# Kernel tuning notes

Hardware: AMD Instinct MI355X
Metric: run time of the kernel (lower is better)

Reference implementation:

```python
import jax, jax.numpy as jnp
import numpy as np

B, T, H, NH, L, V, FF = 2, 1024, 1024, 16, 6, 8192, 4096
D = H // NH
EPS = 1e-5


def _ln(x, g, b):
    mu = jnp.mean(x, axis=-1, keepdims=True)
    var = jnp.mean(jnp.square(x - mu), axis=-1, keepdims=True)
    return (x - mu) * jax.lax.rsqrt(var + EPS) * g + b


def setup_inputs() -> dict:
    key = jax.random.key(0)
    ks = jax.random.split(key, 12)
    s = 1.0 / np.sqrt(H)
    return {
        "x": jax.random.randint(ks[0], (B, T), 0, V),
        "tok_emb": jax.random.normal(ks[1], (V, H), jnp.float32) * s,
        "pos_emb": jax.random.normal(ks[2], (1, T, H), jnp.float32) * s,
        "Wq": jax.random.normal(ks[3], (L, H, H), jnp.float32) * s,
        "bq": jnp.zeros((L, H), jnp.float32),
        "Wk": jax.random.normal(ks[4], (L, H, H), jnp.float32) * s,
        "bk": jnp.zeros((L, H), jnp.float32),
        "Wv": jax.random.normal(ks[5], (L, H, H), jnp.float32) * s,
        "bv": jnp.zeros((L, H), jnp.float32),
        "Wo": jax.random.normal(ks[6], (L, H, H), jnp.float32) * s,
        "bo": jnp.zeros((L, H), jnp.float32),
        "W1": jax.random.normal(ks[7], (L, H, FF), jnp.float32) * s,
        "b1": jnp.zeros((L, FF), jnp.float32),
        "W2": jax.random.normal(ks[8], (L, FF, H), jnp.float32) * (1.0 / np.sqrt(FF)),
        "b2": jnp.zeros((L, H), jnp.float32),
        "ln1_g": jnp.ones((L, H), jnp.float32),
        "ln1_b": jnp.zeros((L, H), jnp.float32),
        "ln2_g": jnp.ones((L, H), jnp.float32),
        "ln2_b": jnp.zeros((L, H), jnp.float32),
        "lnf_g": jnp.ones((H,), jnp.float32),
        "lnf_b": jnp.zeros((H,), jnp.float32),
        "headW": jax.random.normal(ks[9], (H, V), jnp.float32) * s,
        "headb": jnp.zeros((V,), jnp.float32),
    }


def _transformer(x, tok_emb, pos_emb, Wq, bq, Wk, bk, Wv, bv, Wo, bo,
                 W1, b1, W2, b2, ln1_g, ln1_b, ln2_g, ln2_b, lnf_g, lnf_b,
                 headW, headb):
    Tcur = x.shape[1]
    h = tok_emb[x] + pos_emb[:, :Tcur, :]            # [B,T,H]
    mask = jnp.tril(jnp.ones((Tcur, Tcur), bool))    # causal [T,T]
    scale = 1.0 / np.sqrt(D)

    def block(h, p):
        (wq, q_b, wk, k_b, wv, v_b, wo, o_b,
         w1, b1_, w2, b2_, g1, be1, g2, be2) = p
        q = (h @ wq + q_b).reshape(B, Tcur, NH, D)
        k = (h @ wk + k_b).reshape(B, Tcur, NH, D)
        v = (h @ wv + v_b).reshape(B, Tcur, NH, D)
        att = jnp.einsum('bqnd,bknd->bnqk', q, k) * scale
        att = jnp.where(mask, att, -jnp.inf)
        w = jax.nn.softmax(att, axis=-1)
        o = jnp.einsum('bnqk,bknd->bqnd', w, v).reshape(B, Tcur, H)
        h = _ln(h + (o @ wo + o_b), g1, be1)          # post-LN after attention
        m = jax.nn.gelu(h @ w1 + b1_, approximate=False) @ w2 + b2_
        h = _ln(h + m, g2, be2)                       # post-LN after MLP
        return h, None

    params = (Wq, bq, Wk, bk, Wv, bv, Wo, bo, W1, b1, W2, b2,
              ln1_g, ln1_b, ln2_g, ln2_b)
    h, _ = jax.lax.scan(block, h, params)
    h = _ln(h, lnf_g, lnf_b)
    return h @ headW + headb                          # [B,T,V]


def reference(x, tok_emb, pos_emb, Wq, bq, Wk, bk, Wv, bv, Wo, bo,
              W1, b1, W2, b2, ln1_g, ln1_b, ln2_g, ln2_b, lnf_g, lnf_b,
              headW, headb):
    return _transformer(x, tok_emb, pos_emb, Wq, bq, Wk, bk, Wv, bv, Wo, bo,
                        W1, b1, W2, b2, ln1_g, ln1_b, ln2_g, ln2_b,
                        lnf_g, lnf_b, headW, headb)
```

## Files before the change

### kernel.cpp

```cpp
#include <hip/hip_runtime.h>
#include <hip/hip_bf16.h>

#define DEV __device__ __forceinline__

typedef unsigned short u16;
typedef __attribute__((ext_vector_type(8))) short bf16x8;
typedef __attribute__((ext_vector_type(4))) float f32x4;

static constexpr int MB_ = 2;
static constexpr int T_  = 1024;
static constexpr int H_  = 1024;
static constexpr int NH_ = 16;
static constexpr int L_  = 6;
static constexpr int V_  = 8192;
static constexpr int FF_ = 4096;
static constexpr int M_  = MB_ * T_;
static constexpr int QKVN = 3 * H_;

DEV u16 f2bf(float x) {
  __hip_bfloat16 h = __float2bfloat16(x);
  return *reinterpret_cast<u16*>(&h);
}

__global__ __launch_bounds__(256) void embed_kernel(
    const int* __restrict__ x, const float* __restrict__ tok,
    const float* __restrict__ pos, float* __restrict__ h, u16* __restrict__ hb)
{
  int i = blockIdx.x;
  int t = threadIdx.x;
  int id = x[i];
  int tt = i & (T_ - 1);
  float4 a = *(const float4*)(tok + (size_t)id * H_ + t * 4);
  float4 b = *(const float4*)(pos + (size_t)tt * H_ + t * 4);
  float4 r = make_float4(a.x + b.x, a.y + b.y, a.z + b.z, a.w + b.w);
  *(float4*)(h + (size_t)i * H_ + t * 4) = r;
  ushort4 u = make_ushort4(f2bf(r.x), f2bf(r.y), f2bf(r.z), f2bf(r.w));
  *(ushort4*)(hb + (size_t)i * H_ + t * 4) = u;
}

DEV void transpose_tile(const float* __restrict__ W, u16* __restrict__ WT, int R, int C)
{
  __shared__ float Ts[64][65];
  int bx = blockIdx.x, by = blockIdx.y;
  if (bx * 64 >= C || by * 64 >= R) return;
  int r0 = by * 64, c0 = bx * 64;
  int t = threadIdx.x;
  int lr = t >> 4;
  int lcq = (t & 15) * 4;
  #pragma unroll
  for (int it = 0; it < 4; ++it) {
    int r = it * 16 + lr;
    float4 v = *(const float4*)(W + (size_t)(r0 + r) * C + c0 + lcq);
    Ts[r][lcq + 0] = v.x; Ts[r][lcq + 1] = v.y;
    Ts[r][lcq + 2] = v.z; Ts[r][lcq + 3] = v.w;
  }
  __syncthreads();
  #pragma unroll
  for (int it = 0; it < 4; ++it) {
    int n = it * 16 + lr;
    ushort4 u = make_ushort4(f2bf(Ts[lcq + 0][n]), f2bf(Ts[lcq + 1][n]),
                             f2bf(Ts[lcq + 2][n]), f2bf(Ts[lcq + 3][n]));
    *(ushort4*)(WT + (size_t)(c0 + n) * R + r0 + lcq) = u;
  }
}

__global__ __launch_bounds__(256) void transpose_one(
    const float* __restrict__ W, u16* __restrict__ WT, int R, int C)
{ transpose_tile(W, WT, R, C); }

__global__ __launch_bounds__(256) void transpose_layer6(
    const float* __restrict__ Wq, const float* __restrict__ Wk,
    const float* __restrict__ Wv, const float* __restrict__ Wo,
    const float* __restrict__ W1, const float* __restrict__ W2,
    u16* qT, u16* kT, u16* vT, u16* oT, u16* w1T, u16* w2T)
{
  int z = blockIdx.z;
  const float* W; u16* WT; int R, C;
  switch (z) {
    case 0: W = Wq; WT = qT;  R = H_;  C = H_;  break;
    case 1: W = Wk; WT = kT;  R = H_;  C = H_;  break;
    case 2: W = Wv; WT = vT;  R = H_;  C = H_;  break;
    case 3: W = Wo; WT = oT;  R = H_;  C = H_;  break;
    case 4: W = W1; WT = w1T; R = H_;  C = FF_; break;
    default:W = W2; WT = w2T; R = FF_; C = H_;  break;
  }
  transpose_tile(W, WT, R, C);
}

__global__ __launch_bounds__(256) void concat_qkv_bias(
    const float* __restrict__ bq, const float* __restrict__ bk,
    const float* __restrict__ bv, float* __restrict__ outb)
{
  int l = blockIdx.x;
  for (int j = threadIdx.x; j < H_; j += 256) {
    outb[(size_t)l * QKVN + j]          = bq[(size_t)l * H_ + j];
    outb[(size_t)l * QKVN + H_ + j]     = bk[(size_t)l * H_ + j];
    outb[(size_t)l * QKVN + 2 * H_ + j] = bv[(size_t)l * H_ + j];
  }
}


#define GLOAD_LDS16(g, l)                                              \
  __builtin_amdgcn_global_load_lds(                                    \
      (const __attribute__((address_space(1))) void*)(g),              \
      (__attribute__((address_space(3))) void*)(l), 16, 0, 0)

DEV void stage_t(const u16* __restrict__ G, int ldk, int r0g, int kofs,
                 u16* lds, int w, int lane)
{
  const int rr = lane >> 2;
  #pragma unroll
  for (int j = 0; j < 2; ++j) {
    const int row0 = w * 32 + j * 16;
    const int row = row0 + rr;
    const int c = (lane & 3) ^ (row & 3);
    const u16* g = G + (size_t)(r0g + row) * ldk + kofs + c * 8;
    GLOAD_LDS16(g, lds + row0 * 32);
  }
}

DEV bf16x8 frag3(const u16* lds, int rr, int ch) {
  return *(const bf16x8*)(lds + rr * 32 + ((ch ^ (rr & 3)) * 8));
}

template<int N>
DEV void wait_vm_barrier() {
  asm volatile("s_waitcnt vmcnt(%0)" :: "n"(N) : "memory");
  __builtin_amdgcn_s_barrier();
}

DEV void comp3(const u16* As, const u16* Bs, f32x4 (&acc)[4][4],
               int wr, int wc, int lc, int lg)
{
  bf16x8 af[4], bv[4];
  #pragma unroll
  for (int mi = 0; mi < 4; ++mi)
    af[mi] = frag3(As, wr * 64 + mi * 16 + lc, lg);
  #pragma unroll
  for (int ni = 0; ni < 4; ++ni)
    bv[ni] = frag3(Bs, wc * 64 + ni * 16 + lc, lg);
  #pragma unroll
  for (int mi = 0; mi < 4; ++mi)
    #pragma unroll
    for (int ni = 0; ni < 4; ++ni)
      acc[mi][ni] = __builtin_amdgcn_mfma_f32_16x16x32_bf16(af[mi], bv[ni], acc[mi][ni], 0, 0, 0);
}

template<bool PARTIAL, bool DO_GELU, bool WF, bool WB>
__global__ __launch_bounds__(256, 2) void gemm3(
    const u16* __restrict__ A, const u16* __restrict__ BT,
    const float* __restrict__ bias, float* __restrict__ Cf,
    u16* __restrict__ Cb, float* __restrict__ P, int N, int K, int Ksub)
{
  __shared__ __align__(16) u16 As[4][128][32];
  __shared__ __align__(16) u16 Bs[4][128][32];

  const int tid = threadIdx.x;
  const int lane = tid & 63, w = tid >> 6;
  const int wr = w >> 1, wc = w & 1;
  const int lc = lane & 15, lg = lane >> 4;
  const int m0 = blockIdx.y * 128, n0 = blockIdx.x * 128;
  const int kb = blockIdx.z * Ksub;
  const int NT = Ksub >> 5;

  f32x4 acc[4][4];
  #pragma unroll
  for (int i = 0; i < 4; ++i)
    #pragma unroll
    for (int j = 0; j < 4; ++j) {
      f32x4 z = {0.f, 0.f, 0.f, 0.f};
      acc[i][j] = z;
    }

  auto STG = [&](int t, int b) {
    stage_t(A,  K, m0, kb + t * 32, &As[b][0][0], w, lane);
    stage_t(BT, K, n0, kb + t * 32, &Bs[b][0][0], w, lane);
  };

  STG(0, 0);
  STG(1, 1);
  int t = 0;
  for (; t < NT - 2; ++t) {
    STG(t + 2, (t + 2) & 3);
    wait_vm_barrier<8>();
    comp3(&As[t & 3][0][0], &Bs[t & 3][0][0], acc, wr, wc, lc, lg);
  }
  wait_vm_barrier<4>();
  comp3(&As[t & 3][0][0], &Bs[t & 3][0][0], acc, wr, wc, lc, lg);
  ++t;
  wait_vm_barrier<0>();
  comp3(&As[t & 3][0][0], &Bs[t & 3][0][0], acc, wr, wc, lc, lg);

  const size_t zofs = (size_t)blockIdx.z * M_ * N;
  #pragma unroll
  for (int mi = 0; mi < 4; ++mi) {
    #pragma unroll
    for (int ni = 0; ni < 4; ++ni) {
      int gn = n0 + wc * 64 + ni * 16 + lc;
      float bvv = PARTIAL ? 0.f : bias[gn];
      #pragma unroll
      for (int r = 0; r < 4; ++r) {
        int gm = m0 + wr * 64 + mi * 16 + lg * 4 + r;
        float v = acc[mi][ni][r];
        if (PARTIAL) {
          P[zofs + (size_t)gm * N + gn] = v;
        } else {
          v += bvv;
          if (DO_GELU) v = 0.5f * v * (1.f + erff(v * 0.70710678118654752f));
          if (WF) Cf[(size_t)gm * N + gn] = v;
          if (WB) Cb[(size_t)gm * N + gn] = f2bf(v);
        }
      }
    }
  }
}

__global__ __launch_bounds__(256) void ln_kernel(
    const float* __restrict__ X,
    const float* __restrict__ g, const float* __restrict__ be,
    u16* __restrict__ Hb)
{
  __shared__ float red[8];
  int row = blockIdx.x, t = threadIdx.x;
  int lane = t & 63, w = t >> 6;
  float4 v = *(const float4*)(X + (size_t)row * H_ + t * 4);
  float s = v.x + v.y + v.z + v.w;
  float q = v.x * v.x + v.y * v.y + v.z * v.z + v.w * v.w;
  #pragma unroll
  for (int o = 1; o < 64; o <<= 1) { s += __shfl_xor(s, o); q += __shfl_xor(q, o); }
  if (lane == 0) { red[w] = s; red[4 + w] = q; }
  __syncthreads();
  float S = red[0] + red[1] + red[2] + red[3];
  float Q = red[4] + red[5] + red[6] + red[7];
  float mu  = S * (1.f / H_);
  float var = Q * (1.f / H_) - mu * mu;
  float inv = rsqrtf(var + 1e-5f);
  float4 gv = *(const float4*)(g  + t * 4);
  float4 bv = *(const float4*)(be + t * 4);
  ushort4 u = make_ushort4(f2bf((v.x - mu) * inv * gv.x + bv.x),
                           f2bf((v.y - mu) * inv * gv.y + bv.y),
                           f2bf((v.z - mu) * inv * gv.z + bv.z),
                           f2bf((v.w - mu) * inv * gv.w + bv.w));
  *(ushort4*)(Hb + (size_t)row * H_ + t * 4) = u;
}

__global__ __launch_bounds__(256) void ln2_kernel(
    const float* __restrict__ P, int S,
    const float* __restrict__ bias,
    const float* __restrict__ g, const float* __restrict__ be,
    float* __restrict__ h, u16* __restrict__ hb)
{
  __shared__ float red[8];
  int row = blockIdx.x, t = threadIdx.x;
  int lane = t & 63, w = t >> 6;
  float4 v = *(const float4*)(h + (size_t)row * H_ + t * 4);
  float4 bb = *(const float4*)(bias + t * 4);
  v.x += bb.x; v.y += bb.y; v.z += bb.z; v.w += bb.w;
  for (int s0 = 0; s0 < S; ++s0) {
    float4 p = *(const float4*)(P + (size_t)s0 * M_ * H_ + (size_t)row * H_ + t * 4);
    v.x += p.x; v.y += p.y; v.z += p.z; v.w += p.w;
  }
  float s = v.x + v.y + v.z + v.w;
  float q = v.x * v.x + v.y * v.y + v.z * v.z + v.w * v.w;
  #pragma unroll
  for (int o = 1; o < 64; o <<= 1) { s += __shfl_xor(s, o); q += __shfl_xor(q, o); }
  if (lane == 0) { red[w] = s; red[4 + w] = q; }
  __syncthreads();
  float S1 = red[0] + red[1] + red[2] + red[3];
  float Q1 = red[4] + red[5] + red[6] + red[7];
  float mu  = S1 * (1.f / H_);
  float var = Q1 * (1.f / H_) - mu * mu;
  float inv = rsqrtf(var + 1e-5f);
  float4 gv = *(const float4*)(g  + t * 4);
  float4 bv = *(const float4*)(be + t * 4);
  float o0 = (v.x - mu) * inv * gv.x + bv.x;
  float o1 = (v.y - mu) * inv * gv.y + bv.y;
  float o2 = (v.z - mu) * inv * gv.z + bv.z;
  float o3 = (v.w - mu) * inv * gv.w + bv.w;
  *(float4*)(h + (size_t)row * H_ + t * 4) = make_float4(o0, o1, o2, o3);
  ushort4 u = make_ushort4(f2bf(o0), f2bf(o1), f2bf(o2), f2bf(o3));
  *(ushort4*)(hb + (size_t)row * H_ + t * 4) = u;
}

__global__ __launch_bounds__(256) void attn_kernel(
    const u16* __restrict__ qkv, u16* __restrict__ Og)
{
  __shared__ __align__(16) u16 Ks[2][64][72];
  __shared__ __align__(16) u16 Vs[2][64][72];
  __shared__ __align__(16) u16 QPs[4][16][72];

  const int qb = blockIdx.x;
  const int bh = blockIdx.y;
  const int b = bh >> 4, hh = bh & 15;
  const int q0 = qb * 64;
  const size_t base  = ((size_t)b * T_) * QKVN + (size_t)hh * 64;
  const size_t baseO = ((size_t)b * T_) * H_ + (size_t)hh * 64;

  const int tid = threadIdx.x;
  const int lane = tid & 63, w = tid >> 6;
  const int lc = lane & 15, lg = lane >> 4;

  const int r8 = tid >> 3, d8 = (tid & 7) << 3;
  const int vk = tid & 31, vd = (tid >> 5) << 3;

  u16* Qflat = &QPs[0][0][0];

  bf16x8 kr[2], vr[2];
  #pragma unroll
  for (int i = 0; i < 2; ++i) {
    kr[i] = *(const bf16x8*)(qkv + base + H_ + (size_t)(i * 32 + r8) * QKVN + d8);
    vr[i] = *(const bf16x8*)(qkv + base + 2 * H_ + (size_t)(i * 32 + vk) * QKVN + vd);
  }
  #pragma unroll
  for (int i = 0; i < 2; ++i)
    *(bf16x8*)(Qflat + (size_t)(i * 32 + r8) * 72 + d8) =
      *(const bf16x8*)(qkv + base + (size_t)(q0 + i * 32 + r8) * QKVN + d8);
  #pragma unroll
  for (int i = 0; i < 2; ++i) {
    *(bf16x8*)&Ks[0][i * 32 + r8][d8] = kr[i];
    #pragma unroll
    for (int j = 0; j < 8; ++j) Vs[0][vd + j][i * 32 + vk] = ((const u16*)&vr[i])[j];
  }
  __syncthreads();
  bf16x8 aq0 = *(const bf16x8*)(Qflat + (size_t)(w * 16 + lc) * 72 + lg * 8);
  bf16x8 aq1 = *(const bf16x8*)(Qflat + (size_t)(w * 16 + lc) * 72 + 32 + lg * 8);

  float m_r[4], l_r[4];
  f32x4 oa[4];
  #pragma unroll
  for (int i = 0; i < 4; ++i) {
    m_r[i] = -1e30f; l_r[i] = 0.f;
    f32x4 z = {0.f, 0.f, 0.f, 0.f};
    oa[i] = z;
  }
  const float sc2 = 0.125f * 1.4426950408889634f;

  for (int kv = 0; kv <= qb; ++kv) {
    const int cur = kv & 1, nxt = cur ^ 1;
    if (kv < qb) {
      #pragma unroll
      for (int i = 0; i < 2; ++i) {
        kr[i] = *(const bf16x8*)(qkv + base + H_ + (size_t)((kv + 1) * 64 + i * 32 + r8) * QKVN + d8);
        vr[i] = *(const bf16x8*)(qkv + base + 2 * H_ + (size_t)((kv + 1) * 64 + i * 32 + vk) * QKVN + vd);
      }
    }

    f32x4 sfr[4];
    #pragma unroll
    for (int ni = 0; ni < 4; ++ni) { f32x4 z = {0.f,0.f,0.f,0.f}; sfr[ni] = z; }
    #pragma unroll
    for (int ni = 0; ni < 4; ++ni) {
      bf16x8 bk0 = *(const bf16x8*)&Ks[cur][ni * 16 + lc][lg * 8];
      bf16x8 bk1 = *(const bf16x8*)&Ks[cur][ni * 16 + lc][32 + lg * 8];
      sfr[ni] = __builtin_amdgcn_mfma_f32_16x16x32_bf16(aq0, bk0, sfr[ni], 0, 0, 0);
      sfr[ni] = __builtin_amdgcn_mfma_f32_16x16x32_bf16(aq1, bk1, sfr[ni], 0, 0, 0);
    }
    if (kv == qb) {
      #pragma unroll
      for (int ni = 0; ni < 4; ++ni)
        #pragma unroll
        for (int r = 0; r < 4; ++r)
          if (ni * 16 + lc > w * 16 + lg * 4 + r) sfr[ni][r] = -1e30f;
    }
    #pragma unroll
    for (int r = 0; r < 4; ++r) {
      float pm = fmaxf(fmaxf(sfr[0][r], sfr[1][r]), fmaxf(sfr[2][r], sfr[3][r]));
      pm = fmaxf(pm, __shfl_xor(pm, 1));
      pm = fmaxf(pm, __shfl_xor(pm, 2));
      pm = fmaxf(pm, __shfl_xor(pm, 4));
      pm = fmaxf(pm, __shfl_xor(pm, 8));
      float mn = fmaxf(m_r[r], pm);
      float al = exp2f(sc2 * (m_r[r] - mn));
      m_r[r] = mn; l_r[r] *= al;
      #pragma unroll
      for (int f = 0; f < 4; ++f) oa[f][r] *= al;
      float rs = 0.f;
      #pragma unroll
      for (int ni = 0; ni < 4; ++ni) {
        float p = exp2f(sc2 * (sfr[ni][r] - mn));
        sfr[ni][r] = p; rs += p;
      }
      rs += __shfl_xor(rs, 1); rs += __shfl_xor(rs, 2);
      rs += __shfl_xor(rs, 4); rs += __shfl_xor(rs, 8);
      l_r[r] += rs;
    }
    #pragma unroll
    for (int ni = 0; ni < 4; ++ni)
      #pragma unroll
      for (int r = 0; r < 4; ++r)
        QPs[w][lg * 4 + r][ni * 16 + lc] = f2bf(sfr[ni][r]);
    bf16x8 ap0 = *(const bf16x8*)&QPs[w][lc][lg * 8];
    bf16x8 ap1 = *(const bf16x8*)&QPs[w][lc][32 + lg * 8];
    #pragma unroll
    for (int f = 0; f < 4; ++f) {
      bf16x8 bv0 = *(const bf16x8*)&Vs[cur][f * 16 + lc][lg * 8];
      bf16x8 bv1 = *(const bf16x8*)&Vs[cur][f * 16 + lc][32 + lg * 8];
      oa[f] = __builtin_amdgcn_mfma_f32_16x16x32_bf16(ap0, bv0, oa[f], 0, 0, 0);
      oa[f] = __builtin_amdgcn_mfma_f32_16x16x32_bf16(ap1, bv1, oa[f], 0, 0, 0);
    }

    if (kv < qb) {
      #pragma unroll
      for (int i = 0; i < 2; ++i) {
        *(bf16x8*)&Ks[nxt][i * 32 + r8][d8] = kr[i];
        #pragma unroll
        for (int j = 0; j < 8; ++j) Vs[nxt][vd + j][i * 32 + vk] = ((const u16*)&vr[i])[j];
      }
      __syncthreads();
    }
  }

  #pragma unroll
  for (int r = 0; r < 4; ++r) {
    float inv = 1.f / l_r[r];
    int grow = q0 + w * 16 + lg * 4 + r;
    #pragma unroll
    for (int f = 0; f < 4; ++f)
      Og[baseO + (size_t)grow * H_ + f * 16 + lc] = f2bf(oa[f][r] * inv);
  }
}

extern "C" void kernel_launch(void* const* d_in, const int* in_sizes, int n_in,
                              void* d_out, int out_size, void* d_ws, size_t ws_size,
                              hipStream_t stream)
{
  const int*   x    = (const int*)  d_in[0];
  const float* tok  = (const float*)d_in[1];
  const float* pos  = (const float*)d_in[2];
  const float* Wq   = (const float*)d_in[3];
  const float* bq   = (const float*)d_in[4];
  const float* Wk   = (const float*)d_in[5];
  const float* bk   = (const float*)d_in[6];
  const float* Wv   = (const float*)d_in[7];
  const float* bv   = (const float*)d_in[8];
  const float* Wo   = (const float*)d_in[9];
  const float* bo   = (const float*)d_in[10];
  const float* W1   = (const float*)d_in[11];
  const float* b1   = (const float*)d_in[12];
  const float* W2   = (const float*)d_in[13];
  const float* b2   = (const float*)d_in[14];
  const float* g1   = (const float*)d_in[15];
  const float* be1  = (const float*)d_in[16];
  const float* g2   = (const float*)d_in[17];
  const float* be2  = (const float*)d_in[18];
  const float* gf   = (const float*)d_in[19];
  const float* bef  = (const float*)d_in[20];
  const float* hW   = (const float*)d_in[21];
  const float* hbias= (const float*)d_in[22];
  float* out = (float*)d_out;

  char* wsp = (char*)d_ws;
  size_t off = 0;
  auto alloc = [&](size_t bytes) -> void* {
    void* p = wsp + off;
    off += (bytes + 255) & ~(size_t)255;
    return p;
  };
  float* h    = (float*)alloc((size_t)M_ * H_ * 4);
  u16*   hb   = (u16*)  alloc((size_t)M_ * H_ * 2);
  u16*   qkv  = (u16*)  alloc((size_t)M_ * QKVN * 2);
  u16*   ob_  = (u16*)  alloc((size_t)M_ * H_ * 2);
  u16*   m1   = (u16*)  alloc((size_t)M_ * FF_ * 2);
  float* P    = (float*)alloc((size_t)4 * M_ * H_ * 4);
  u16*   hT   = (u16*)P;
  u16*   qkvT = (u16*)  alloc((size_t)QKVN * H_ * 2);
  u16*   oT   = (u16*)  alloc((size_t)H_ * H_ * 2);
  u16*   w1T  = (u16*)  alloc((size_t)H_ * FF_ * 2);
  u16*   w2T  = (u16*)  alloc((size_t)FF_ * H_ * 2);
  float* bqkv = (float*)alloc((size_t)L_ * QKVN * 4);
  (void)in_sizes; (void)n_in; (void)out_size; (void)ws_size;

  embed_kernel<<<M_, 256, 0, stream>>>(x, tok, pos, h, hb);
  concat_qkv_bias<<<L_, 256, 0, stream>>>(bq, bk, bv, bqkv);

  for (int l = 0; l < L_; ++l) {
    transpose_layer6<<<dim3(64, 64, 6), 256, 0, stream>>>(
        Wq + (size_t)l * H_ * H_, Wk + (size_t)l * H_ * H_,
        Wv + (size_t)l * H_ * H_, Wo + (size_t)l * H_ * H_,
        W1 + (size_t)l * H_ * FF_, W2 + (size_t)l * FF_ * H_,
        qkvT, qkvT + (size_t)H_ * H_, qkvT + 2 * (size_t)H_ * H_,
        oT, w1T, w2T);
    gemm3<false, false, false, true><<<dim3(QKVN / 128, M_ / 128, 1), 256, 0, stream>>>(
        hb, qkvT, bqkv + (size_t)l * QKVN, nullptr, qkv, nullptr, QKVN, H_, H_);
    attn_kernel<<<dim3(T_ / 64, MB_ * NH_), 256, 0, stream>>>(qkv, ob_);
    gemm3<true, false, false, false><<<dim3(H_ / 128, M_ / 128, 2), 256, 0, stream>>>(
        ob_, oT, nullptr, nullptr, nullptr, P, H_, H_, H_ / 2);
    ln2_kernel<<<M_, 256, 0, stream>>>(P, 2, bo + l * H_, g1 + l * H_, be1 + l * H_, h, hb);
    gemm3<false, true, false, true><<<dim3(FF_ / 128, M_ / 128, 1), 256, 0, stream>>>(
        hb, w1T, b1 + (size_t)l * FF_, nullptr, m1, nullptr, FF_, H_, H_);
    gemm3<true, false, false, false><<<dim3(H_ / 128, M_ / 128, 4), 256, 0, stream>>>(
        m1, w2T, nullptr, nullptr, nullptr, P, H_, FF_, FF_ / 4);
    ln2_kernel<<<M_, 256, 0, stream>>>(P, 4, b2 + l * H_, g2 + l * H_, be2 + l * H_, h, hb);
  }

  ln_kernel<<<M_, 256, 0, stream>>>(h, gf, bef, hb);
  transpose_one<<<dim3(V_ / 64, H_ / 64), 256, 0, stream>>>(hW, hT, H_, V_);
  gemm3<false, false, true, false><<<dim3(V_ / 128, M_ / 128, 1), 256, 0, stream>>>(
      hb, hT, hbias, out, nullptr, nullptr, V_, H_, H_);
}
```

Baseline: 1.123 ms.

## Fuse fp32 weight transpose and bf16 conversion into GEMM B-operand loading

Removes the separate per-layer weight transpose/convert kernels. The GEMM now reads fp32 weights directly from global memory into registers, converts them to bf16 and writes them transposed into a padded LDS tile, double-buffered in registers across k-steps. This saves the extra kernel launches and the write-then-reread of bf16 transposed weights. In exchange, each tile now loads fp32 weights, which doubles B-operand traffic, and adds register pressure. The weights are also re-read and re-converted by every row-block instead of once.

```diff
diff --git a/kernel.cpp b/kernel.cpp
--- a/kernel.cpp
+++ b/kernel.cpp
@@ -38,55 +38,6 @@
   *(ushort4*)(hb + (size_t)i * H_ + t * 4) = u;
 }
 
-DEV void transpose_tile(const float* __restrict__ W, u16* __restrict__ WT, int R, int C)
-{
-  __shared__ float Ts[64][65];
-  int bx = blockIdx.x, by = blockIdx.y;
-  if (bx * 64 >= C || by * 64 >= R) return;
-  int r0 = by * 64, c0 = bx * 64;
-  int t = threadIdx.x;
-  int lr = t >> 4;
-  int lcq = (t & 15) * 4;
-  #pragma unroll
-  for (int it = 0; it < 4; ++it) {
-    int r = it * 16 + lr;
-    float4 v = *(const float4*)(W + (size_t)(r0 + r) * C + c0 + lcq);
-    Ts[r][lcq + 0] = v.x; Ts[r][lcq + 1] = v.y;
-    Ts[r][lcq + 2] = v.z; Ts[r][lcq + 3] = v.w;
-  }
-  __syncthreads();
-  #pragma unroll
-  for (int it = 0; it < 4; ++it) {
-    int n = it * 16 + lr;
-    ushort4 u = make_ushort4(f2bf(Ts[lcq + 0][n]), f2bf(Ts[lcq + 1][n]),
-                             f2bf(Ts[lcq + 2][n]), f2bf(Ts[lcq + 3][n]));
-    *(ushort4*)(WT + (size_t)(c0 + n) * R + r0 + lcq) = u;
-  }
-}
-
-__global__ __launch_bounds__(256) void transpose_one(
-    const float* __restrict__ W, u16* __restrict__ WT, int R, int C)
-{ transpose_tile(W, WT, R, C); }
-
-__global__ __launch_bounds__(256) void transpose_layer6(
-    const float* __restrict__ Wq, const float* __restrict__ Wk,
-    const float* __restrict__ Wv, const float* __restrict__ Wo,
-    const float* __restrict__ W1, const float* __restrict__ W2,
-    u16* qT, u16* kT, u16* vT, u16* oT, u16* w1T, u16* w2T)
-{
-  int z = blockIdx.z;
-  const float* W; u16* WT; int R, C;
-  switch (z) {
-    case 0: W = Wq; WT = qT;  R = H_;  C = H_;  break;
-    case 1: W = Wk; WT = kT;  R = H_;  C = H_;  break;
-    case 2: W = Wv; WT = vT;  R = H_;  C = H_;  break;
-    case 3: W = Wo; WT = oT;  R = H_;  C = H_;  break;
-    case 4: W = W1; WT = w1T; R = H_;  C = FF_; break;
-    default:W = W2; WT = w2T; R = FF_; C = H_;  break;
-  }
-  transpose_tile(W, WT, R, C);
-}
-
 __global__ __launch_bounds__(256) void concat_qkv_bias(
     const float* __restrict__ bq, const float* __restrict__ bk,
     const float* __restrict__ bv, float* __restrict__ outb)
@@ -123,13 +74,43 @@
   return *(const bf16x8*)(lds + rr * 32 + ((ch ^ (rr & 3)) * 8));
 }
 
-template<int N>
-DEV void wait_vm_barrier() {
-  asm volatile("s_waitcnt vmcnt(%0)" :: "n"(N) : "memory");
-  __builtin_amdgcn_s_barrier();
-}
-
-DEV void comp3(const u16* As, const u16* Bs, f32x4 (&acc)[4][4],
+DEV bf16x8 fragB(const u16* lds, int rr, int ch) {
+  return *(const bf16x8*)(lds + rr * 40 + ch * 8);
+}
+
+DEV void loadB(const float* __restrict__ Bseg, int ldn, int ncol, int k0,
+               int w, int lane, float (&br)[16])
+{
+  #pragma unroll
+  for (int nh = 0; nh < 2; ++nh)
+    #pragma unroll
+    for (int kq = 0; kq < 2; ++kq)
+      #pragma unroll
+      for (int kc = 0; kc < 4; ++kc)
+        br[nh * 8 + kq * 4 + kc] =
+          Bseg[(size_t)(k0 + w * 8 + kq * 4 + kc) * ldn + ncol + nh * 64 + lane];
+}
+
+DEV void writeB(u16* Bsbuf, int w, int lane, const float (&br)[16])
+{
+  #pragma unroll
+  for (int nh = 0; nh < 2; ++nh) {
+    int n = nh * 64 + lane;
+    #pragma unroll
+    for (int kq = 0; kq < 2; ++kq) {
+      unsigned b0 = f2bf(br[nh * 8 + kq * 4 + 0]);
+      unsigned b1 = f2bf(br[nh * 8 + kq * 4 + 1]);
+      unsigned b2 = f2bf(br[nh * 8 + kq * 4 + 2]);
+      unsigned b3 = f2bf(br[nh * 8 + kq * 4 + 3]);
+      uint2 pk;
+      pk.x = b0 | (b1 << 16);
+      pk.y = b2 | (b3 << 16);
+      *(uint2*)(Bsbuf + n * 40 + w * 8 + kq * 4) = pk;
+    }
+  }
+}
+
+DEV void comp5(const u16* As, const u16* Bs, f32x4 (&acc)[4][4],
                int wr, int wc, int lc, int lg)
 {
   bf16x8 af[4], bv[4];
@@ -138,7 +119,7 @@
     af[mi] = frag3(As, wr * 64 + mi * 16 + lc, lg);
   #pragma unroll
   for (int ni = 0; ni < 4; ++ni)
-    bv[ni] = frag3(Bs, wc * 64 + ni * 16 + lc, lg);
+    bv[ni] = fragB(Bs, wc * 64 + ni * 16 + lc, lg);
   #pragma unroll
   for (int mi = 0; mi < 4; ++mi)
     #pragma unroll
@@ -147,19 +128,24 @@
 }
 
 template<bool PARTIAL, bool DO_GELU, bool WF, bool WB>
-__global__ __launch_bounds__(256, 2) void gemm3(
-    const u16* __restrict__ A, const u16* __restrict__ BT,
+__global__ __launch_bounds__(256, 2) void gemm5(
+    const u16* __restrict__ A,
+    const float* __restrict__ B0, const float* __restrict__ B1,
+    const float* __restrict__ B2, int segsh, int ldn,
     const float* __restrict__ bias, float* __restrict__ Cf,
     u16* __restrict__ Cb, float* __restrict__ P, int N, int K, int Ksub)
 {
   __shared__ __align__(16) u16 As[4][128][32];
-  __shared__ __align__(16) u16 Bs[4][128][32];
+  __shared__ __align__(16) u16 Bs[4][128][40];
 
   const int tid = threadIdx.x;
   const int lane = tid & 63, w = tid >> 6;
   const int wr = w >> 1, wc = w & 1;
   const int lc = lane & 15, lg = lane >> 4;
   const int m0 = blockIdx.y * 128, n0 = blockIdx.x * 128;
+  const int seg = n0 >> segsh;
+  const float* Bseg = (seg == 0) ? B0 : ((seg == 1) ? B1 : B2);
+  const int ncol = n0 & ((1 << segsh) - 1);
   const int kb = blockIdx.z * Ksub;
   const int NT = Ksub >> 5;
 
@@ -172,24 +158,36 @@
       acc[i][j] = z;
     }
 
-  auto STG = [&](int t, int b) {
-    stage_t(A,  K, m0, kb + t * 32, &As[b][0][0], w, lane);
-    stage_t(BT, K, n0, kb + t * 32, &Bs[b][0][0], w, lane);
-  };
-
-  STG(0, 0);
-  STG(1, 1);
+  float brA[16], brB[16];
+  loadB(Bseg, ldn, ncol, kb, w, lane, brA);
+  stage_t(A, K, m0, kb, &As[0][0][0], w, lane);
+  loadB(Bseg, ldn, ncol, kb + 32, w, lane, brB);
+  stage_t(A, K, m0, kb + 32, &As[1][0][0], w, lane);
+  asm volatile("s_waitcnt vmcnt(20)" ::: "memory");
+  writeB(&Bs[0][0][0], w, lane, brA);
+
   int t = 0;
-  for (; t < NT - 2; ++t) {
-    STG(t + 2, (t + 2) & 3);
-    wait_vm_barrier<8>();
-    comp3(&As[t & 3][0][0], &Bs[t & 3][0][0], acc, wr, wc, lc, lg);
-  }
-  wait_vm_barrier<4>();
-  comp3(&As[t & 3][0][0], &Bs[t & 3][0][0], acc, wr, wc, lc, lg);
-  ++t;
-  wait_vm_barrier<0>();
-  comp3(&As[t & 3][0][0], &Bs[t & 3][0][0], acc, wr, wc, lc, lg);
+  for (; t + 3 < NT; t += 2) {
+    loadB(Bseg, ldn, ncol, kb + (t + 2) * 32, w, lane, brA);
+    stage_t(A, K, m0, kb + (t + 2) * 32, &As[(t + 2) & 3][0][0], w, lane);
+    asm volatile("s_waitcnt vmcnt(20) lgkmcnt(0)" ::: "memory");
+    __builtin_amdgcn_s_barrier();
+    writeB(&Bs[(t + 1) & 3][0][0], w, lane, brB);
+    comp5(&As[t & 3][0][0], &Bs[t & 3][0][0], acc, wr, wc, lc, lg);
+    loadB(Bseg, ldn, ncol, kb + (t + 3) * 32, w, lane, brB);
+    stage_t(A, K, m0, kb + (t + 3) * 32, &As[(t + 3) & 3][0][0], w, lane);
+    asm volatile("s_waitcnt vmcnt(20) lgkmcnt(0)" ::: "memory");
+    __builtin_amdgcn_s_barrier();
+    writeB(&Bs[(t + 2) & 3][0][0], w, lane, brA);
+    comp5(&As[(t + 1) & 3][0][0], &Bs[(t + 1) & 3][0][0], acc, wr, wc, lc, lg);
+  }
+  asm volatile("s_waitcnt vmcnt(2) lgkmcnt(0)" ::: "memory");
+  __builtin_amdgcn_s_barrier();
+  writeB(&Bs[(NT - 1) & 3][0][0], w, lane, brB);
+  comp5(&As[(NT - 2) & 3][0][0], &Bs[(NT - 2) & 3][0][0], acc, wr, wc, lc, lg);
+  asm volatile("s_waitcnt vmcnt(0) lgkmcnt(0)" ::: "memory");
+  __builtin_amdgcn_s_barrier();
+  comp5(&As[(NT - 1) & 3][0][0], &Bs[(NT - 1) & 3][0][0], acc, wr, wc, lc, lg);
 
   const size_t zofs = (size_t)blockIdx.z * M_ * N;
   #pragma unroll
@@ -462,11 +460,6 @@
   u16*   ob_  = (u16*)  alloc((size_t)M_ * H_ * 2);
   u16*   m1   = (u16*)  alloc((size_t)M_ * FF_ * 2);
   float* P    = (float*)alloc((size_t)4 * M_ * H_ * 4);
-  u16*   hT   = (u16*)P;
-  u16*   qkvT = (u16*)  alloc((size_t)QKVN * H_ * 2);
-  u16*   oT   = (u16*)  alloc((size_t)H_ * H_ * 2);
-  u16*   w1T  = (u16*)  alloc((size_t)H_ * FF_ * 2);
-  u16*   w2T  = (u16*)  alloc((size_t)FF_ * H_ * 2);
   float* bqkv = (float*)alloc((size_t)L_ * QKVN * 4);
   (void)in_sizes; (void)n_in; (void)out_size; (void)ws_size;
 
@@ -474,27 +467,26 @@
   concat_qkv_bias<<<L_, 256, 0, stream>>>(bq, bk, bv, bqkv);
 
   for (int l = 0; l < L_; ++l) {
-    transpose_layer6<<<dim3(64, 64, 6), 256, 0, stream>>>(
-        Wq + (size_t)l * H_ * H_, Wk + (size_t)l * H_ * H_,
-        Wv + (size_t)l * H_ * H_, Wo + (size_t)l * H_ * H_,
-        W1 + (size_t)l * H_ * FF_, W2 + (size_t)l * FF_ * H_,
-        qkvT, qkvT + (size_t)H_ * H_, qkvT + 2 * (size_t)H_ * H_,
-        oT, w1T, w2T);
-    gemm3<false, false, false, true><<<dim3(QKVN / 128, M_ / 128, 1), 256, 0, stream>>>(
-        hb, qkvT, bqkv + (size_t)l * QKVN, nullptr, qkv, nullptr, QKVN, H_, H_);
+    const float* wq = Wq + (size_t)l * H_ * H_;
+    const float* wk = Wk + (size_t)l * H_ * H_;
+    const float* wv = Wv + (size_t)l * H_ * H_;
+    const float* wo = Wo + (size_t)l * H_ * H_;
+    const float* w1 = W1 + (size_t)l * H_ * FF_;
+    const float* w2 = W2 + (size_t)l * FF_ * H_;
+    gemm5<false, false, false, true><<<dim3(QKVN / 128, M_ / 128, 1), 256, 0, stream>>>(
+        hb, wq, wk, wv, 10, H_, bqkv + (size_t)l * QKVN, nullptr, qkv, nullptr, QKVN, H_, H_);
     attn_kernel<<<dim3(T_ / 64, MB_ * NH_), 256, 0, stream>>>(qkv, ob_);
-    gemm3<true, false, false, false><<<dim3(H_ / 128, M_ / 128, 2), 256, 0, stream>>>(
-        ob_, oT, nullptr, nullptr, nullptr, P, H_, H_, H_ / 2);
+    gemm5<true, false, false, false><<<dim3(H_ / 128, M_ / 128, 2), 256, 0, stream>>>(
+        ob_, wo, wo, wo, 30, H_, nullptr, nullptr, nullptr, P, H_, H_, H_ / 2);
     ln2_kernel<<<M_, 256, 0, stream>>>(P, 2, bo + l * H_, g1 + l * H_, be1 + l * H_, h, hb);
-    gemm3<false, true, false, true><<<dim3(FF_ / 128, M_ / 128, 1), 256, 0, stream>>>(
-        hb, w1T, b1 + (size_t)l * FF_, nullptr, m1, nullptr, FF_, H_, H_);
-    gemm3<true, false, false, false><<<dim3(H_ / 128, M_ / 128, 4), 256, 0, stream>>>(
-        m1, w2T, nullptr, nullptr, nullptr, P, H_, FF_, FF_ / 4);
+    gemm5<false, true, false, true><<<dim3(FF_ / 128, M_ / 128, 1), 256, 0, stream>>>(
+        hb, w1, w1, w1, 30, FF_, b1 + (size_t)l * FF_, nullptr, m1, nullptr, FF_, H_, H_);
+    gemm5<true, false, false, false><<<dim3(H_ / 128, M_ / 128, 4), 256, 0, stream>>>(
+        m1, w2, w2, w2, 30, H_, nullptr, nullptr, nullptr, P, H_, FF_, FF_ / 4);
     ln2_kernel<<<M_, 256, 0, stream>>>(P, 4, b2 + l * H_, g2 + l * H_, be2 + l * H_, h, hb);
   }
 
   ln_kernel<<<M_, 256, 0, stream>>>(h, gf, bef, hb);
-  transpose_one<<<dim3(V_ / 64, H_ / 64), 256, 0, stream>>>(hW, hT, H_, V_);
-  gemm3<false, false, true, false><<<dim3(V_ / 128, M_ / 128, 1), 256, 0, stream>>>(
-      hb, hT, hbias, out, nullptr, nullptr, V_, H_, H_);
-}
+  gemm5<false, false, true, false><<<dim3(V_ / 128, M_ / 128, 1), 256, 0, stream>>>(
+      hb, hW, hW, hW, 30, V_, hbias, out, nullptr, nullptr, V_, H_, H_);
+}
```

After: 1.216 ms. 8.3% more time.

## Use 3-stage GEMM LDS ring with XCD tile remap and reversed attention order

Applied to the files above, without the earlier changes.

The GEMM LDS ring buffer shrinks from four stages to three so three workgroups can share a CU (launch bounds 2→3). The wait and barrier now come before issuing the next stage load. Workgroup IDs are remapped so that consecutive tiles land on the same XCD, which should improve L2 reuse. The attention kernel launches query blocks in reverse, so the longest causal blocks start first and load balance improves. The risk is less prefetch depth, register pressure from the higher occupancy target, and a vmcnt(4) wait with only one stage in flight possibly stalling.

```diff
diff --git a/kernel.cpp b/kernel.cpp
--- a/kernel.cpp
+++ b/kernel.cpp
@@ -123,12 +123,6 @@
   return *(const bf16x8*)(lds + rr * 32 + ((ch ^ (rr & 3)) * 8));
 }
 
-template<int N>
-DEV void wait_vm_barrier() {
-  asm volatile("s_waitcnt vmcnt(%0)" :: "n"(N) : "memory");
-  __builtin_amdgcn_s_barrier();
-}
-
 DEV void comp3(const u16* As, const u16* Bs, f32x4 (&acc)[4][4],
                int wr, int wc, int lc, int lg)
 {
@@ -147,19 +141,27 @@
 }
 
 template<bool PARTIAL, bool DO_GELU, bool WF, bool WB>
-__global__ __launch_bounds__(256, 2) void gemm3(
+__global__ __launch_bounds__(256, 3) void gemm3(
     const u16* __restrict__ A, const u16* __restrict__ BT,
     const float* __restrict__ bias, float* __restrict__ Cf,
     u16* __restrict__ Cb, float* __restrict__ P, int N, int K, int Ksub)
 {
-  __shared__ __align__(16) u16 As[4][128][32];
-  __shared__ __align__(16) u16 Bs[4][128][32];
+  __shared__ __align__(16) u16 As[3][128][32];
+  __shared__ __align__(16) u16 Bs[3][128][32];
 
   const int tid = threadIdx.x;
   const int lane = tid & 63, w = tid >> 6;
   const int wr = w >> 1, wc = w & 1;
   const int lc = lane & 15, lg = lane >> 4;
-  const int m0 = blockIdx.y * 128, n0 = blockIdx.x * 128;
+
+  const int gx = gridDim.x;
+  const int nwg = gx * gridDim.y;
+  const int lid = blockIdx.y * gx + blockIdx.x;
+  const int q8 = nwg >> 3, r8s = nwg & 7;
+  const int xcd = lid & 7, ord = lid >> 3;
+  const int sid = (xcd < r8s ? xcd * (q8 + 1) : r8s * (q8 + 1) + (xcd - r8s) * q8) + ord;
+  const int m0 = (sid / gx) * 128, n0 = (sid % gx) * 128;
+
   const int kb = blockIdx.z * Ksub;
   const int NT = Ksub >> 5;
 
@@ -181,15 +183,18 @@
   STG(1, 1);
   int t = 0;
   for (; t < NT - 2; ++t) {
-    STG(t + 2, (t + 2) & 3);
-    wait_vm_barrier<8>();
-    comp3(&As[t & 3][0][0], &Bs[t & 3][0][0], acc, wr, wc, lc, lg);
-  }
-  wait_vm_barrier<4>();
-  comp3(&As[t & 3][0][0], &Bs[t & 3][0][0], acc, wr, wc, lc, lg);
+    asm volatile("s_waitcnt vmcnt(4)" ::: "memory");
+    __builtin_amdgcn_s_barrier();
+    STG(t + 2, (t + 2) % 3);
+    comp3(&As[t % 3][0][0], &Bs[t % 3][0][0], acc, wr, wc, lc, lg);
+  }
+  asm volatile("s_waitcnt vmcnt(4)" ::: "memory");
+  __builtin_amdgcn_s_barrier();
+  comp3(&As[t % 3][0][0], &Bs[t % 3][0][0], acc, wr, wc, lc, lg);
   ++t;
-  wait_vm_barrier<0>();
-  comp3(&As[t & 3][0][0], &Bs[t & 3][0][0], acc, wr, wc, lc, lg);
+  asm volatile("s_waitcnt vmcnt(0)" ::: "memory");
+  __builtin_amdgcn_s_barrier();
+  comp3(&As[t % 3][0][0], &Bs[t % 3][0][0], acc, wr, wc, lc, lg);
 
   const size_t zofs = (size_t)blockIdx.z * M_ * N;
   #pragma unroll
@@ -289,7 +294,7 @@
   __shared__ __align__(16) u16 Vs[2][64][72];
   __shared__ __align__(16) u16 QPs[4][16][72];
 
-  const int qb = blockIdx.x;
+  const int qb = gridDim.x - 1 - blockIdx.x;
   const int bh = blockIdx.y;
   const int b = bh >> 4, hh = bh & 15;
   const int q0 = qb * 64;
```

Result: slower. 1.169 ms (+4.0%).
